# Performance work log

Hardware: AMD Instinct MI355X
Metric: run time of the kernel (lower is better)

Reference implementation:

```python
import jax, jax.numpy as jnp
import numpy as np

EPS_NORM = 1e-12
EPS_ENT = 1e-12
TEMPERATURE = 0.5
CONTRAST_DENOM = 128.0 * 100.0


def _l2_normalize(x, axis=-1):
    n = jnp.linalg.norm(x, axis=axis, keepdims=True)
    return x / jnp.maximum(n, EPS_NORM)


def setup_inputs() -> dict:
    key0 = jax.random.key(0)
    k1, k2, k3, k4 = jax.random.split(key0, 4)
    B, L, C = 16, 2048, 512
    M = 512
    return {
        "key": jax.random.normal(k1, (B, L, C), dtype=jnp.float32),
        "query": jax.random.normal(k2, (B, L, C), dtype=jnp.float32),
        "keys": jax.random.uniform(k3, (M, C), dtype=jnp.float32),
        "values": jax.random.uniform(k4, (M, C), dtype=jnp.float32),
        "mode": 0,
    }


def reference(key, query, keys, values, mode):
    B, L, C = key.shape
    k = _l2_normalize(key.reshape(-1, C))    # [T, C]
    q = _l2_normalize(query.reshape(-1, C))  # [T, C]

    # --- gatheringLoss ---
    score = jnp.einsum('tc,mc->tm', k, keys)            # [T, M]
    # top-1 of softmax(score) == argmax(score) (softmax is monotone)
    idx = jnp.argmax(score, axis=1)                     # [T]
    nearest_values = values[idx]                        # [T, C]
    gathering_loss = jnp.mean((q - nearest_values) ** 2)

    logits = score / TEMPERATURE                        # [T, M]
    logp = jax.nn.log_softmax(logits, axis=-1)
    gathered = jnp.take_along_axis(logp, idx[:, None], axis=1)  # [T, 1]
    contrast_loss = jnp.sum(gathered) / (-CONTRAST_DENOM)

    # --- read ---
    weights = jax.nn.softmax(score, axis=-1)            # [T, M]
    # EntropyLoss: mean over rows of -sum(w * log(w + eps))
    entropy_loss = jnp.mean(-jnp.sum(weights * jnp.log(weights + EPS_ENT), axis=-1))
    read_query = weights @ values                       # [T, C]

    return (read_query.reshape(B, L, C), entropy_loss, gathering_loss,
            contrast_loss, keys, values)
```

## Files before the change

### kernel.cpp

```cpp
#include <hip/hip_runtime.h>

typedef short short8 __attribute__((ext_vector_type(8)));
typedef float floatx4 __attribute__((ext_vector_type(4)));

#define C_DIM 512
#define KQ_STRIDE 1040

__device__ __forceinline__ unsigned short f2bf(float f) {
    unsigned u = __builtin_bit_cast(unsigned, f);
    u = u + 0x7fffu + ((u >> 16) & 1u);
    return (unsigned short)(u >> 16);
}

__device__ __forceinline__ unsigned skey(float s, int col) {
    unsigned u = __builtin_bit_cast(unsigned, s);
    u = ((int)u < 0) ? ~u : (u | 0x80000000u);
    return (u & ~0x1FFu) | (unsigned)(511 - col);
}

template <int CTRL>
__device__ __forceinline__ float dppAddF(float x) {
    int t = __builtin_amdgcn_update_dpp(0, __builtin_bit_cast(int, x), CTRL, 0xF, 0xF, true);
    return x + __builtin_bit_cast(float, t);
}
template <int CTRL>
__device__ __forceinline__ unsigned dppMaxU(unsigned x) {
    unsigned u = (unsigned)__builtin_amdgcn_update_dpp(0, (int)x, CTRL, 0xF, 0xF, true);
    return u > x ? u : x;
}
__device__ __forceinline__ float rowAdd16(float x) {
    x = dppAddF<0xB1>(x);
    x = dppAddF<0x4E>(x);
    x = dppAddF<0x124>(x);
    x = dppAddF<0x128>(x);
    return x;
}

__global__ __launch_bounds__(256) void pack_kernel(
    const float* __restrict__ keys, const float* __restrict__ values,
    unsigned short* __restrict__ keysFrag, unsigned short* __restrict__ valsFrag,
    float* __restrict__ keysOut, float* __restrict__ valsOut,
    float* __restrict__ scal) {
    int tid = blockIdx.x * 256 + threadIdx.x;
    if (tid < 65536) {
        int e  = tid & 32767;
        int l  = e & 63;
        int NT = (e >> 6) & 31;
        int kt = e >> 11;
        int li = l & 15, q4 = l >> 4;
        unsigned short tmp[8];
        if (tid < 32768) {
            const float* s = keys + (size_t)(NT * 16 + li) * C_DIM + kt * 32 + q4 * 8;
#pragma unroll
            for (int j = 0; j < 8; j++) tmp[j] = f2bf(s[j]);
            unsigned short* d = keysFrag + ((size_t)(kt * 32 + NT) * 64 + l) * 8;
            *(ushort4*)d       = make_ushort4(tmp[0], tmp[1], tmp[2], tmp[3]);
            *(ushort4*)(d + 4) = make_ushort4(tmp[4], tmp[5], tmp[6], tmp[7]);
        } else {
#pragma unroll
            for (int j = 0; j < 8; j++)
                tmp[j] = f2bf(values[(size_t)(kt * 32 + q4 * 8 + j) * C_DIM + NT * 16 + li]);
            unsigned short* d = valsFrag + ((size_t)(kt * 32 + NT) * 64 + l) * 8;
            *(ushort4*)d       = make_ushort4(tmp[0], tmp[1], tmp[2], tmp[3]);
            *(ushort4*)(d + 4) = make_ushort4(tmp[4], tmp[5], tmp[6], tmp[7]);
        }
    } else {
        int ct = tid - 65536;
        if (ct == 0) { scal[0] = 0.f; scal[1] = 0.f; scal[2] = 0.f; }
#pragma unroll
        for (int i = 0; i < 4; i++) {
            int idx = ct + i * 32768;
            if (idx < 65536) ((float4*)keysOut)[idx] = ((const float4*)keys)[idx];
            else             ((float4*)valsOut)[idx - 65536] = ((const float4*)values)[idx - 65536];
        }
    }
}

__global__ __launch_bounds__(512, 4) void fused_kernel(
    const float* __restrict__ key,
    const float* __restrict__ query,
    const unsigned short* __restrict__ keysFrag,
    const unsigned short* __restrict__ valsFrag,
    const float* __restrict__ values,
    float* __restrict__ outRQ,
    float* __restrict__ scal) {
    __shared__ char kq[64 * KQ_STRIDE];
    __shared__ __align__(16) float stats[8][64][4];
    __shared__ float gpart[8];

    const int tid = threadIdx.x;
    const int w  = tid >> 6;
    const int l  = tid & 63;
    const int li = l & 15;
    const int q4 = l >> 4;
    const int row0 = blockIdx.x << 6;

    const float* qtb = query + (size_t)row0 * C_DIM;
    float tch0 = qtb[(tid * 2) * 32];
    float tch1 = qtb[(tid * 2 + 1) * 32];

#pragma unroll
    for (int it = 0; it < 2; it++) {
        int r = (w << 3) + (it << 2) + q4;
        const float4* src = (const float4*)(key + (size_t)(row0 + r) * C_DIM);
        float4 v[8];
        float ss = 0.f;
#pragma unroll
        for (int i = 0; i < 8; i++) {
            v[i] = src[i * 16 + li];
            ss += v[i].x * v[i].x + v[i].y * v[i].y + v[i].z * v[i].z + v[i].w * v[i].w;
        }
        ss = rowAdd16(ss);
        float inv = 1.0f / fmaxf(sqrtf(ss), 1e-12f);
        char* dstrow = kq + r * KQ_STRIDE;
#pragma unroll
        for (int i = 0; i < 8; i++) {
            ushort4 b = make_ushort4(f2bf(v[i].x * inv), f2bf(v[i].y * inv),
                                     f2bf(v[i].z * inv), f2bf(v[i].w * inv));
            *(ushort4*)(dstrow + i * 128 + li * 8) = b;
        }
    }
    asm volatile("" :: "v"(tch0), "v"(tch1));
    __syncthreads();

    floatx4 acc1[16];
#pragma unroll
    for (int i = 0; i < 16; i++) acc1[i] = (floatx4){0.f, 0.f, 0.f, 0.f};
    {
        const short8* kf = (const short8*)keysFrag;
        short8 bcur[4], bnxt[4];
#pragma unroll
        for (int nt = 0; nt < 4; nt++) bcur[nt] = kf[(size_t)((w * 4 + nt) * 64 + l)];
        for (int kt = 0; kt < 16; kt++) {
            if (kt < 15) {
#pragma unroll
                for (int nt = 0; nt < 4; nt++)
                    bnxt[nt] = kf[(size_t)(((kt + 1) * 32 + w * 4 + nt) * 64 + l)];
            }
            short8 a[4];
#pragma unroll
            for (int rg = 0; rg < 4; rg++)
                a[rg] = *(const short8*)(kq + (rg * 16 + li) * KQ_STRIDE + kt * 64 + q4 * 16);
#pragma unroll
            for (int rg = 0; rg < 4; rg++)
#pragma unroll
                for (int nt = 0; nt < 4; nt++)
                    acc1[rg * 4 + nt] = __builtin_amdgcn_mfma_f32_16x16x32_bf16(
                        a[rg], bcur[nt], acc1[rg * 4 + nt], 0, 0, 0);
#pragma unroll
            for (int nt = 0; nt < 4; nt++) bcur[nt] = bnxt[nt];
        }
    }

#pragma unroll
    for (int rg = 0; rg < 4; rg++) {
#pragma unroll
        for (int reg = 0; reg < 4; reg++) {
            const int colbase = (w << 6) + li;
            float s0 = acc1[rg * 4 + 0][reg];
            float s1 = acc1[rg * 4 + 1][reg];
            float s2 = acc1[rg * 4 + 2][reg];
            float s3 = acc1[rg * 4 + 3][reg];
            unsigned K  = skey(s0, colbase);
            unsigned K1 = skey(s1, colbase + 16);
            unsigned K2 = skey(s2, colbase + 32);
            unsigned K3 = skey(s3, colbase + 48);
            K = K1 > K ? K1 : K;
            K = K2 > K ? K2 : K;
            K = K3 > K ? K3 : K;
            float p0 = __expf(s0), p1 = __expf(s1), p2 = __expf(s2), p3 = __expf(s3);
            float z1 = (p0 + p1) + (p2 + p3);
            float e1 = p0 * s0 + p1 * s1 + p2 * s2 + p3 * s3;
            float z2 = p0 * p0 + p1 * p1 + p2 * p2 + p3 * p3;
            acc1[rg * 4 + 0][reg] = p0;
            acc1[rg * 4 + 1][reg] = p1;
            acc1[rg * 4 + 2][reg] = p2;
            acc1[rg * 4 + 3][reg] = p3;
            K = dppMaxU<0xB1>(K);  z1 = dppAddF<0xB1>(z1);  e1 = dppAddF<0xB1>(e1);  z2 = dppAddF<0xB1>(z2);
            K = dppMaxU<0x4E>(K);  z1 = dppAddF<0x4E>(z1);  e1 = dppAddF<0x4E>(e1);  z2 = dppAddF<0x4E>(z2);
            K = dppMaxU<0x124>(K); z1 = dppAddF<0x124>(z1); e1 = dppAddF<0x124>(e1); z2 = dppAddF<0x124>(z2);
            K = dppMaxU<0x128>(K); z1 = dppAddF<0x128>(z1); e1 = dppAddF<0x128>(e1); z2 = dppAddF<0x128>(z2);
            if (li == 0) {
                floatx4 sv;
                sv[0] = __builtin_bit_cast(float, K);
                sv[1] = z1; sv[2] = e1; sv[3] = z2;
                *(floatx4*)stats[w][rg * 16 + q4 * 4 + reg] = sv;
            }
        }
    }
    __syncthreads();

#pragma unroll
    for (int rg = 0; rg < 4; rg++) {
#pragma unroll
        for (int reg = 0; reg < 4; reg++) {
            int r = rg * 16 + q4 * 4 + reg;
#pragma unroll
            for (int nt = 0; nt < 4; nt++) {
                int col = (w << 6) + nt * 16 + li;
                *(unsigned short*)(kq + r * KQ_STRIDE + col * 2) = f2bf(acc1[rg * 4 + nt][reg]);
            }
        }
    }
    __syncthreads();

    floatx4 acc2[16];
#pragma unroll
    for (int i = 0; i < 16; i++) acc2[i] = (floatx4){0.f, 0.f, 0.f, 0.f};
    {
        const short8* vf = (const short8*)valsFrag;
        short8 bcur[4], bnxt[4];
#pragma unroll
        for (int nt = 0; nt < 4; nt++) bcur[nt] = vf[(size_t)((w * 4 + nt) * 64 + l)];
        for (int kt = 0; kt < 16; kt++) {
            if (kt < 15) {
#pragma unroll
                for (int nt = 0; nt < 4; nt++)
                    bnxt[nt] = vf[(size_t)(((kt + 1) * 32 + w * 4 + nt) * 64 + l)];
            }
            short8 a[4];
#pragma unroll
            for (int rg = 0; rg < 4; rg++)
                a[rg] = *(const short8*)(kq + (rg * 16 + li) * KQ_STRIDE + kt * 64 + q4 * 16);
#pragma unroll
            for (int rg = 0; rg < 4; rg++)
#pragma unroll
                for (int nt = 0; nt < 4; nt++)
                    acc2[rg * 4 + nt] = __builtin_amdgcn_mfma_f32_16x16x32_bf16(
                        a[rg], bcur[nt], acc2[rg * 4 + nt], 0, 0, 0);
#pragma unroll
            for (int nt = 0; nt < 4; nt++) bcur[nt] = bnxt[nt];
        }
    }

    unsigned K; float z1, e1, z2;
    {
        floatx4 v = *(const floatx4*)stats[0][l];
        K = __builtin_bit_cast(unsigned, v[0]); z1 = v[1]; e1 = v[2]; z2 = v[3];
#pragma unroll
        for (int p = 1; p < 8; p++) {
            floatx4 u = *(const floatx4*)stats[p][l];
            unsigned Ko = __builtin_bit_cast(unsigned, u[0]);
            K = Ko > K ? Ko : K;
            z1 += u[1]; e1 += u[2]; z2 += u[3];
        }
    }
    const float iz = 1.0f / z1;
    const int myidx = 511 - (int)(K & 0x1FFu);

#pragma unroll
    for (int rg = 0; rg < 4; rg++) {
#pragma unroll
        for (int reg = 0; reg < 4; reg++) {
            int r = rg * 16 + q4 * 4 + reg;
            float izr = __shfl(iz, r, 64);
            float* orow = outRQ + (size_t)(row0 + r) * C_DIM + (w << 6) + li;
#pragma unroll
            for (int nt = 0; nt < 4; nt++) orow[nt * 16] = acc2[rg * 4 + nt][reg] * izr;
        }
    }

    float gacc = 0.f;
#pragma unroll
    for (int rr = 0; rr < 8; rr++) {
        int r = (w << 3) + rr;
        int idxr = __shfl(myidx, r, 64);
        const float4* qr = (const float4*)(query + (size_t)(row0 + r) * C_DIM);
        float4 a = qr[l * 2], b = qr[l * 2 + 1];
        float ss = a.x * a.x + a.y * a.y + a.z * a.z + a.w * a.w +
                   b.x * b.x + b.y * b.y + b.z * b.z + b.w * b.w;
        ss = rowAdd16(ss);
        ss += __shfl_xor(ss, 16, 64);
        ss += __shfl_xor(ss, 32, 64);
        float inv = 1.0f / fmaxf(sqrtf(ss), 1e-12f);
        const float4* vr = (const float4*)(values + (size_t)idxr * C_DIM);
        float4 va = vr[l * 2], vb = vr[l * 2 + 1];
        float d;
        d = a.x * inv - va.x; gacc += d * d;
        d = a.y * inv - va.y; gacc += d * d;
        d = a.z * inv - va.z; gacc += d * d;
        d = a.w * inv - va.w; gacc += d * d;
        d = b.x * inv - vb.x; gacc += d * d;
        d = b.y * inv - vb.y; gacc += d * d;
        d = b.z * inv - vb.z; gacc += d * d;
        d = b.w * inv - vb.w; gacc += d * d;
    }
    gacc = rowAdd16(gacc);
    gacc += __shfl_xor(gacc, 16, 64);
    gacc += __shfl_xor(gacc, 32, 64);
    if (l == 0) gpart[w] = gacc;

    if (w == 0) {
        unsigned um = (K >> 31) ? (K & 0x7FFFFFFFu) : ~K;
        um &= ~0x1FFu;
        float m1 = __builtin_bit_cast(float, um);
        float ent = __logf(z1) - e1 * iz;
        float con = __logf(z2) - 2.0f * m1;
#pragma unroll
        for (int msk = 1; msk < 64; msk <<= 1) {
            ent += __shfl_xor(ent, msk, 64);
            con += __shfl_xor(con, msk, 64);
        }
        if (l == 0) {
            atomicAdd(&scal[0], ent * (1.0f / 32768.0f));
            atomicAdd(&scal[2], con * (1.0f / 12800.0f));
        }
    }
    __syncthreads();
    if (tid == 0) {
        float s = 0.f;
#pragma unroll
        for (int i = 0; i < 8; i++) s += gpart[i];
        atomicAdd(&scal[1], s * (1.0f / (32768.0f * 512.0f)));
    }
}

extern "C" void kernel_launch(void* const* d_in, const int* in_sizes, int n_in,
                              void* d_out, int out_size, void* d_ws, size_t ws_size,
                              hipStream_t stream) {
    (void)in_sizes; (void)n_in; (void)out_size; (void)ws_size;
    const float* key    = (const float*)d_in[0];
    const float* query  = (const float*)d_in[1];
    const float* keysIn = (const float*)d_in[2];
    const float* valsIn = (const float*)d_in[3];
    float* out = (float*)d_out;

    unsigned short* keysFrag = (unsigned short*)d_ws;
    unsigned short* valsFrag = keysFrag + 512 * 512;

    float* outRQ   = out;
    float* scal    = out + 16777216;
    float* keysOut = out + 16777219;
    float* valsOut = keysOut + 262144;

    pack_kernel<<<384, 256, 0, stream>>>(keysIn, valsIn, keysFrag, valsFrag,
                                         keysOut, valsOut, scal);
    fused_kernel<<<512, 512, 0, stream>>>(key, query, keysFrag, valsFrag, valsIn, outRQ, scal);
}
```

Measured before the change: 239.9 us.

## Double rows per block to 128 to reuse key/value fragments across more rows

Each block now processes 128 token rows instead of 64, with 256 blocks instead of 512, so every keys/values bf16 fragment loaded from global memory feeds twice as many MFMAs. Accumulator arrays double to 32 floatx4 each, launch bounds drop to 2 blocks per CU, and LDS use doubles. The per-row stats reduction is split into two halves (A/B) because each lane now covers two rows. This trades occupancy and register pressure, with a possible risk of spills, for fewer global fragment reloads. With only 256 blocks on a device of this size, it also leaves less parallelism to spread across the CUs.

```diff
diff --git a/kernel.cpp b/kernel.cpp
--- a/kernel.cpp
+++ b/kernel.cpp
@@ -5,6 +5,7 @@
 
 #define C_DIM 512
 #define KQ_STRIDE 1040
+#define ROWS 128
 
 __device__ __forceinline__ unsigned short f2bf(float f) {
     unsigned u = __builtin_bit_cast(unsigned, f);
@@ -76,7 +77,7 @@
     }
 }
 
-__global__ __launch_bounds__(512, 4) void fused_kernel(
+__global__ __launch_bounds__(512, 2) void fused_kernel(
     const float* __restrict__ key,
     const float* __restrict__ query,
     const unsigned short* __restrict__ keysFrag,
@@ -84,8 +85,8 @@
     const float* __restrict__ values,
     float* __restrict__ outRQ,
     float* __restrict__ scal) {
-    __shared__ char kq[64 * KQ_STRIDE];
-    __shared__ __align__(16) float stats[8][64][4];
+    __shared__ char kq[ROWS * KQ_STRIDE];
+    __shared__ __align__(16) float stats[8][ROWS][4];
     __shared__ float gpart[8];
 
     const int tid = threadIdx.x;
@@ -93,15 +94,17 @@
     const int l  = tid & 63;
     const int li = l & 15;
     const int q4 = l >> 4;
-    const int row0 = blockIdx.x << 6;
+    const int row0 = blockIdx.x << 7;
 
     const float* qtb = query + (size_t)row0 * C_DIM;
-    float tch0 = qtb[(tid * 2) * 32];
-    float tch1 = qtb[(tid * 2 + 1) * 32];
-
-#pragma unroll
-    for (int it = 0; it < 2; it++) {
-        int r = (w << 3) + (it << 2) + q4;
+    float tch0 = qtb[(tid)        * 32];
+    float tch1 = qtb[(tid +  512) * 32];
+    float tch2 = qtb[(tid + 1024) * 32];
+    float tch3 = qtb[(tid + 1536) * 32];
+
+#pragma unroll
+    for (int it = 0; it < 4; it++) {
+        int r = (w << 4) + (it << 2) + q4;
         const float4* src = (const float4*)(key + (size_t)(row0 + r) * C_DIM);
         float4 v[8];
         float ss = 0.f;
@@ -120,12 +123,12 @@
             *(ushort4*)(dstrow + i * 128 + li * 8) = b;
         }
     }
-    asm volatile("" :: "v"(tch0), "v"(tch1));
+    asm volatile("" :: "v"(tch0), "v"(tch1), "v"(tch2), "v"(tch3));
     __syncthreads();
 
-    floatx4 acc1[16];
-#pragma unroll
-    for (int i = 0; i < 16; i++) acc1[i] = (floatx4){0.f, 0.f, 0.f, 0.f};
+    floatx4 acc1[32];
+#pragma unroll
+    for (int i = 0; i < 32; i++) acc1[i] = (floatx4){0.f, 0.f, 0.f, 0.f};
     {
         const short8* kf = (const short8*)keysFrag;
         short8 bcur[4], bnxt[4];
@@ -137,12 +140,12 @@
                 for (int nt = 0; nt < 4; nt++)
                     bnxt[nt] = kf[(size_t)(((kt + 1) * 32 + w * 4 + nt) * 64 + l)];
             }
-            short8 a[4];
-#pragma unroll
-            for (int rg = 0; rg < 4; rg++)
+            short8 a[8];
+#pragma unroll
+            for (int rg = 0; rg < 8; rg++)
                 a[rg] = *(const short8*)(kq + (rg * 16 + li) * KQ_STRIDE + kt * 64 + q4 * 16);
 #pragma unroll
-            for (int rg = 0; rg < 4; rg++)
+            for (int rg = 0; rg < 8; rg++)
 #pragma unroll
                 for (int nt = 0; nt < 4; nt++)
                     acc1[rg * 4 + nt] = __builtin_amdgcn_mfma_f32_16x16x32_bf16(
@@ -153,7 +156,7 @@
     }
 
 #pragma unroll
-    for (int rg = 0; rg < 4; rg++) {
+    for (int rg = 0; rg < 8; rg++) {
 #pragma unroll
         for (int reg = 0; reg < 4; reg++) {
             const int colbase = (w << 6) + li;
@@ -191,7 +194,7 @@
     __syncthreads();
 
 #pragma unroll
-    for (int rg = 0; rg < 4; rg++) {
+    for (int rg = 0; rg < 8; rg++) {
 #pragma unroll
         for (int reg = 0; reg < 4; reg++) {
             int r = rg * 16 + q4 * 4 + reg;
@@ -204,9 +207,9 @@
     }
     __syncthreads();
 
-    floatx4 acc2[16];
-#pragma unroll
-    for (int i = 0; i < 16; i++) acc2[i] = (floatx4){0.f, 0.f, 0.f, 0.f};
+    floatx4 acc2[32];
+#pragma unroll
+    for (int i = 0; i < 32; i++) acc2[i] = (floatx4){0.f, 0.f, 0.f, 0.f};
     {
         const short8* vf = (const short8*)valsFrag;
         short8 bcur[4], bnxt[4];
@@ -218,12 +221,12 @@
                 for (int nt = 0; nt < 4; nt++)
                     bnxt[nt] = vf[(size_t)(((kt + 1) * 32 + w * 4 + nt) * 64 + l)];
             }
-            short8 a[4];
-#pragma unroll
-            for (int rg = 0; rg < 4; rg++)
+            short8 a[8];
+#pragma unroll
+            for (int rg = 0; rg < 8; rg++)
                 a[rg] = *(const short8*)(kq + (rg * 16 + li) * KQ_STRIDE + kt * 64 + q4 * 16);
 #pragma unroll
-            for (int rg = 0; rg < 4; rg++)
+            for (int rg = 0; rg < 8; rg++)
 #pragma unroll
                 for (int nt = 0; nt < 4; nt++)
                     acc2[rg * 4 + nt] = __builtin_amdgcn_mfma_f32_16x16x32_bf16(
@@ -233,27 +236,33 @@
         }
     }
 
-    unsigned K; float z1, e1, z2;
+    unsigned KA, KB; float z1A, e1A, z2A, z1B, e1B, z2B;
     {
-        floatx4 v = *(const floatx4*)stats[0][l];
-        K = __builtin_bit_cast(unsigned, v[0]); z1 = v[1]; e1 = v[2]; z2 = v[3];
+        floatx4 vA = *(const floatx4*)stats[0][l];
+        floatx4 vB = *(const floatx4*)stats[0][64 + l];
+        KA = __builtin_bit_cast(unsigned, vA[0]); z1A = vA[1]; e1A = vA[2]; z2A = vA[3];
+        KB = __builtin_bit_cast(unsigned, vB[0]); z1B = vB[1]; e1B = vB[2]; z2B = vB[3];
 #pragma unroll
         for (int p = 1; p < 8; p++) {
-            floatx4 u = *(const floatx4*)stats[p][l];
-            unsigned Ko = __builtin_bit_cast(unsigned, u[0]);
-            K = Ko > K ? Ko : K;
-            z1 += u[1]; e1 += u[2]; z2 += u[3];
-        }
-    }
-    const float iz = 1.0f / z1;
-    const int myidx = 511 - (int)(K & 0x1FFu);
-
-#pragma unroll
-    for (int rg = 0; rg < 4; rg++) {
+            floatx4 uA = *(const floatx4*)stats[p][l];
+            floatx4 uB = *(const floatx4*)stats[p][64 + l];
+            unsigned KoA = __builtin_bit_cast(unsigned, uA[0]);
+            unsigned KoB = __builtin_bit_cast(unsigned, uB[0]);
+            KA = KoA > KA ? KoA : KA; z1A += uA[1]; e1A += uA[2]; z2A += uA[3];
+            KB = KoB > KB ? KoB : KB; z1B += uB[1]; e1B += uB[2]; z2B += uB[3];
+        }
+    }
+    const float izA = 1.0f / z1A;
+    const float izB = 1.0f / z1B;
+    const int idxA = 511 - (int)(KA & 0x1FFu);
+    const int idxB = 511 - (int)(KB & 0x1FFu);
+
+#pragma unroll
+    for (int rg = 0; rg < 8; rg++) {
 #pragma unroll
         for (int reg = 0; reg < 4; reg++) {
             int r = rg * 16 + q4 * 4 + reg;
-            float izr = __shfl(iz, r, 64);
+            float izr = (rg < 4) ? __shfl(izA, r & 63, 64) : __shfl(izB, r & 63, 64);
             float* orow = outRQ + (size_t)(row0 + r) * C_DIM + (w << 6) + li;
 #pragma unroll
             for (int nt = 0; nt < 4; nt++) orow[nt * 16] = acc2[rg * 4 + nt][reg] * izr;
@@ -262,9 +271,9 @@
 
     float gacc = 0.f;
 #pragma unroll
-    for (int rr = 0; rr < 8; rr++) {
-        int r = (w << 3) + rr;
-        int idxr = __shfl(myidx, r, 64);
+    for (int rr = 0; rr < 16; rr++) {
+        int r = (w << 4) + rr;
+        int idxr = __shfl((w < 4) ? idxA : idxB, r & 63, 64);
         const float4* qr = (const float4*)(query + (size_t)(row0 + r) * C_DIM);
         float4 a = qr[l * 2], b = qr[l * 2 + 1];
         float ss = a.x * a.x + a.y * a.y + a.z * a.z + a.w * a.w +
@@ -291,11 +300,13 @@
     if (l == 0) gpart[w] = gacc;
 
     if (w == 0) {
-        unsigned um = (K >> 31) ? (K & 0x7FFFFFFFu) : ~K;
-        um &= ~0x1FFu;
-        float m1 = __builtin_bit_cast(float, um);
-        float ent = __logf(z1) - e1 * iz;
-        float con = __logf(z2) - 2.0f * m1;
+        unsigned umA = (KA >> 31) ? (KA & 0x7FFFFFFFu) : ~KA;
+        unsigned umB = (KB >> 31) ? (KB & 0x7FFFFFFFu) : ~KB;
+        umA &= ~0x1FFu; umB &= ~0x1FFu;
+        float m1A = __builtin_bit_cast(float, umA);
+        float m1B = __builtin_bit_cast(float, umB);
+        float ent = (__logf(z1A) - e1A * izA) + (__logf(z1B) - e1B * izB);
+        float con = (__logf(z2A) - 2.0f * m1A) + (__logf(z2B) - 2.0f * m1B);
 #pragma unroll
         for (int msk = 1; msk < 64; msk <<= 1) {
             ent += __shfl_xor(ent, msk, 64);
@@ -335,5 +346,5 @@
 
     pack_kernel<<<384, 256, 0, stream>>>(keysIn, valsIn, keysFrag, valsFrag,
                                          keysOut, valsOut, scal);
-    fused_kernel<<<512, 512, 0, stream>>>(key, query, keysFrag, valsFrag, valsIn, outRQ, scal);
-}
+    fused_kernel<<<256, 512, 0, stream>>>(key, query, keysFrag, valsFrag, valsIn, outRQ, scal);
+}
```

Result: no change. 235.7 us (-1.7%).
